# Performance work log

Hardware: AMD Instinct MI355X
Metric: run time of the kernel (lower is better)

Reference implementation:

```python
import jax, jax.numpy as jnp
import numpy as np

S = 2048      # total tokens
DIM = 1024    # model dim
H = 16        # attention heads
DH = 64       # head dim
BOT = 256     # bottleneck dim
NIMG = 4      # images (equal size)
L = S // NIMG # tokens per image
K = 256       # sparse_k
IH = 4        # indexer heads
ID = 16       # indexer head dim
MAXREL = 64   # hardcoded in module
NBUCK = 2 * MAXREL + 1
GH = IH * 2   # gate MLP hidden (expansion=2)


def setup_inputs() -> dict:
    key = jax.random.key(0)
    ks = jax.random.split(key, 16)
    r = lambda i, sh, s=0.02: jax.random.normal(ks[i], sh, jnp.float32) * s
    return dict(
        hidden_states=jax.random.normal(ks[0], (S, DIM), jnp.float32),
        patch_coords=jax.random.randint(ks[1], (S, 2), 0, 64, dtype=jnp.int32),
        cu_seqlens=jnp.arange(NIMG + 1, dtype=jnp.int32) * L,
        rotary_pos_emb=jax.random.uniform(ks[2], (S, DH // 2), jnp.float32) * 3.0,
        Wq_idx=r(3, (2 * IH * ID, DIM)),
        Wk_idx=r(4, (2 * IH * ID, DIM)),
        W1g=r(5, (GH, IH)), b1g=jnp.zeros((GH,), jnp.float32),
        W2g=r(6, (IH, GH)), b2g=jnp.zeros((IH,), jnp.float32),
        rpe_table=r(7, (NBUCK, IH)),
        Wqkv_d=r(8, (BOT, DIM)), bqkv_d=jnp.zeros((BOT,), jnp.float32),
        Wqkv_u=r(9, (3 * DIM, BOT)), bqkv_u=jnp.zeros((3 * DIM,), jnp.float32),
        Wp_d=r(10, (BOT, DIM)), bp_d=jnp.zeros((BOT,), jnp.float32),
        Wp_u=r(11, (DIM, BOT)), bp_u=jnp.zeros((DIM,), jnp.float32),
        scaler=jnp.ones((1,), jnp.float32),
    )


def _rotate_half(x):
    x1, x2 = jnp.split(x, 2, axis=-1)
    return jnp.concatenate([-x2, x1], axis=-1)


def reference(hidden_states, patch_coords, cu_seqlens, rotary_pos_emb,
              Wq_idx, Wk_idx, W1g, b1g, W2g, b2g, rpe_table,
              Wqkv_d, bqkv_d, Wqkv_u, bqkv_u, Wp_d, bp_d, Wp_u, bp_u, scaler):
    n = cu_seqlens.shape[0] - 1            # images (equal size L)
    Li = hidden_states.shape[0] // n
    neg = jnp.finfo(hidden_states.dtype).min

    # QKV via low-rank bottleneck
    qkv = (hidden_states @ Wqkv_d.T + bqkv_d) @ Wqkv_u.T + bqkv_u  # [S, 3*DIM]
    qkv = qkv.reshape(S, 3, H, DH)
    q, k, v = qkv[:, 0], qkv[:, 1], qkv[:, 2]                      # [S, H, DH]

    # vision RoPE (emb = cat(rpe, rpe))
    emb = jnp.concatenate([rotary_pos_emb, rotary_pos_emb], axis=-1)  # [S, DH]
    cos = jnp.cos(emb)[:, None, :]
    sin = jnpp if False else jnp.sin(emb)[:, None, :]
    q = q * cos + _rotate_half(q) * sin
    k = k * cos + _rotate_half(k) * sin

    # ---- interaction indexer, vmapped over equal-size images ----
    xs = hidden_states.reshape(n, Li, DIM)
    pos = patch_coords[:, 1].reshape(n, Li).astype(jnp.float32)
    qI = (xs @ Wq_idx.T).reshape(n, Li, 2 * IH, ID)
    kI = (xs @ Wk_idx.T).reshape(n, Li, 2 * IH, ID)
    dot = jnp.einsum('nqhd,nkhd->nqkh', qI, kI)                    # [n, L, L, 2*IH]
    data_in, gate_in = dot[..., :IH], dot[..., IH:]
    rel = jnp.clip(pos[:, :, None] - pos[:, None, :], -MAXREL, MAXREL)
    bucket = (rel + MAXREL).astype(jnp.int32)                      # [n, L, L]
    rpe = rpe_table[bucket]                                        # [n, L, L, IH]
    relu_scores = jax.nn.relu(data_in + rpe)
    g = jax.nn.sigmoid(jax.nn.relu((gate_in + rpe) @ W1g.T + b1g) @ W2g.T + b2g)
    index_scores = (relu_scores * g).sum(-1)                       # [n, L, L]

    # top-k sparse mask (0 at selected keys, -inf-ish elsewhere)
    _, topk_idx = jax.lax.top_k(index_scores, K)                   # [n, L, K]
    ni = jnp.arange(n)[:, None, None]
    ri = jnp.arange(Li)[None, :, None]
    mask_local = jnp.full((n, Li, Li), neg, hidden_states.dtype).at[ni, ri, topk_idx].set(0.0)

    # block-diagonal full mask
    mask = jnp.full((S, S), neg, hidden_states.dtype)
    for i in range(n):
        mask = mask.at[i * Li:(i + 1) * Li, i * Li:(i + 1) * Li].set(mask_local[i])

    # dense SDPA with additive mask
    att = jnp.einsum('qhd,khd->hqk', q, k) / jnp.sqrt(jnp.float32(DH)).astype(q.dtype)
    att = att + mask[None]
    p = jax.nn.softmax(att, axis=-1)
    out = jnp.einsum('hqk,khd->qhd', p, v).reshape(S, H * DH)

    final = (out @ Wp_d.T + bp_d) @ Wp_u.T + bp_u
    return final * scaler
```

## Files before the change

kernel.cpp:

```cpp
#include <hip/hip_runtime.h>
#include <hip/hip_bf16.h>

#define S_    2048
#define DIM_  1024
#define H_    16
#define DH_   64
#define BOT_  256
#define NIMG_ 4
#define LI_   512
#define K_    256
#define IH_   4
#define ID_   16
#define MAXREL_ 64
#define NBUCK_ 129
#define GH_   8
#define IDH2_ 128

typedef short bf16x8 __attribute__((ext_vector_type(8)));
typedef float f32x4  __attribute__((ext_vector_type(4)));

__device__ __forceinline__ unsigned short f2bf(float x) {
    unsigned u = __float_as_uint(x);
    return (unsigned short)((u + 0x7fffu + ((u >> 16) & 1u)) >> 16);
}
__device__ __forceinline__ float bf2f(unsigned short h) {
    return __uint_as_float(((unsigned)h) << 16);
}

#define OFF_W1_    2097152
#define OFF_WQ_    2359296
#define OFF_WK_    2490368
#define OFF_WQKVU_ 2621440
#define OFF_WPD_   3407872
#define OFF_WPU_   3670016
#define NSPLIT_    3932160

__global__ __launch_bounds__(256) void split_all_kernel(
    const float* __restrict__ hid, const float* __restrict__ wqd,
    const float* __restrict__ wq,  const float* __restrict__ wk,
    const float* __restrict__ wqu, const float* __restrict__ wpd,
    const float* __restrict__ wpu,
    unsigned short* __restrict__ hi, unsigned short* __restrict__ lo)
{
    long e = ((long)blockIdx.x * 256 + threadIdx.x) * 4;
    if (e >= NSPLIT_) return;
    const float* src; long off;
    if (e < OFF_W1_)         { src = hid; off = 0; }
    else if (e < OFF_WQ_)    { src = wqd; off = OFF_W1_; }
    else if (e < OFF_WK_)    { src = wq;  off = OFF_WQ_; }
    else if (e < OFF_WQKVU_) { src = wk;  off = OFF_WK_; }
    else if (e < OFF_WPD_)   { src = wqu; off = OFF_WQKVU_; }
    else if (e < OFF_WPU_)   { src = wpd; off = OFF_WPD_; }
    else                     { src = wpu; off = OFF_WPU_; }
    float4 v = *(const float4*)(src + (e - off));
    ushort4 h, l;
    h.x = f2bf(v.x); l.x = f2bf(v.x - bf2f(h.x));
    h.y = f2bf(v.y); l.y = f2bf(v.y - bf2f(h.y));
    h.z = f2bf(v.z); l.z = f2bf(v.z - bf2f(h.z));
    h.w = f2bf(v.w); l.w = f2bf(v.w - bf2f(h.w));
    *(ushort4*)&hi[e] = h;
    *(ushort4*)&lo[e] = l;
}

__global__ __launch_bounds__(256) void gemm_bf16x3(
    const unsigned short* __restrict__ Ah, const unsigned short* __restrict__ Al,
    const unsigned short* __restrict__ Bh, const unsigned short* __restrict__ Bl,
    const float* __restrict__ bias, const float* __restrict__ scale_ptr,
    float* __restrict__ Cf, int M, int N, int Kd)
{
    __shared__ unsigned short sAh[128 * 40], sAl[128 * 40];
    __shared__ unsigned short sBh[64 * 40],  sBl[64 * 40];
    int tid = threadIdx.x;
    int lane = tid & 63, wv = tid >> 6;
    int wr = wv >> 1, wc = wv & 1;
    int row0 = blockIdx.y * 128, col0 = blockIdx.x * 64;

    f32x4 acc[4][2];
#pragma unroll
    for (int i = 0; i < 4; i++)
#pragma unroll
        for (int j = 0; j < 2; j++) acc[i][j] = (f32x4){0.f, 0.f, 0.f, 0.f};

    int ar = tid >> 1, ac = (tid & 1) * 16;
    int br = tid >> 2, bc = (tid & 3) * 8;
    const unsigned short* gAh = Ah + (size_t)(row0 + ar) * Kd + ac;
    const unsigned short* gAl = Al + (size_t)(row0 + ar) * Kd + ac;
    const unsigned short* gBh = Bh + (size_t)(col0 + br) * Kd + bc;
    const unsigned short* gBl = Bl + (size_t)(col0 + br) * Kd + bc;
    int am = lane & 15, qk = (lane >> 4) * 8;

    for (int k0 = 0; k0 < Kd; k0 += 32) {
        __syncthreads();
        *(float4*)&sAh[ar * 40 + ac]     = *(const float4*)(gAh + k0);
        *(float4*)&sAh[ar * 40 + ac + 8] = *(const float4*)(gAh + k0 + 8);
        *(float4*)&sAl[ar * 40 + ac]     = *(const float4*)(gAl + k0);
        *(float4*)&sAl[ar * 40 + ac + 8] = *(const float4*)(gAl + k0 + 8);
        *(float4*)&sBh[br * 40 + bc]     = *(const float4*)(gBh + k0);
        *(float4*)&sBl[br * 40 + bc]     = *(const float4*)(gBl + k0);
        __syncthreads();

        bf16x8 ah[4], al[4], bh[2], bl[2];
#pragma unroll
        for (int rt = 0; rt < 4; rt++) {
            int r = wr * 64 + rt * 16 + am;
            ah[rt] = *(const bf16x8*)&sAh[r * 40 + qk];
            al[rt] = *(const bf16x8*)&sAl[r * 40 + qk];
        }
#pragma unroll
        for (int ct = 0; ct < 2; ct++) {
            int c = wc * 32 + ct * 16 + am;
            bh[ct] = *(const bf16x8*)&sBh[c * 40 + qk];
            bl[ct] = *(const bf16x8*)&sBl[c * 40 + qk];
        }
#pragma unroll
        for (int rt = 0; rt < 4; rt++)
#pragma unroll
            for (int ct = 0; ct < 2; ct++) {
                acc[rt][ct] = __builtin_amdgcn_mfma_f32_16x16x32_bf16(ah[rt], bh[ct], acc[rt][ct], 0, 0, 0);
                acc[rt][ct] = __builtin_amdgcn_mfma_f32_16x16x32_bf16(ah[rt], bl[ct], acc[rt][ct], 0, 0, 0);
                acc[rt][ct] = __builtin_amdgcn_mfma_f32_16x16x32_bf16(al[rt], bh[ct], acc[rt][ct], 0, 0, 0);
            }
    }

    float scl = scale_ptr ? *scale_ptr : 1.0f;
    int rq = (lane >> 4) * 4;
#pragma unroll
    for (int rt = 0; rt < 4; rt++)
#pragma unroll
        for (int ct = 0; ct < 2; ct++) {
            int col = col0 + wc * 32 + ct * 16 + am;
            float bz = bias ? bias[col] : 0.0f;
#pragma unroll
            for (int rg = 0; rg < 4; rg++) {
                int row = row0 + wr * 64 + rt * 16 + rq + rg;
                Cf[(size_t)row * N + col] = (acc[rt][ct][rg] + bz) * scl;
            }
        }
}

__global__ __launch_bounds__(256) void gemm64_bf16x3(
    const unsigned short* __restrict__ Ah, const unsigned short* __restrict__ Al,
    const unsigned short* __restrict__ Bh, const unsigned short* __restrict__ Bl,
    const float* __restrict__ bias_lo, const float* __restrict__ bias_hi,
    float* __restrict__ Cf, unsigned short* __restrict__ Chi,
    unsigned short* __restrict__ Clo, int M, int N, int Kd, int split_col)
{
    __shared__ unsigned short sAh[64 * 40], sAl[64 * 40];
    __shared__ unsigned short sBh[64 * 40], sBl[64 * 40];
    int tid = threadIdx.x;
    int lane = tid & 63, wv = tid >> 6;
    int wr = wv >> 1, wc = wv & 1;
    int row0 = blockIdx.y * 64, col0 = blockIdx.x * 64;

    f32x4 acc[2][2];
#pragma unroll
    for (int i = 0; i < 2; i++)
#pragma unroll
        for (int j = 0; j < 2; j++) acc[i][j] = (f32x4){0.f, 0.f, 0.f, 0.f};

    int sr = tid >> 2, sc = (tid & 3) * 8;
    const unsigned short* gAh = Ah + (size_t)(row0 + sr) * Kd + sc;
    const unsigned short* gAl = Al + (size_t)(row0 + sr) * Kd + sc;
    const unsigned short* gBh = Bh + (size_t)(col0 + sr) * Kd + sc;
    const unsigned short* gBl = Bl + (size_t)(col0 + sr) * Kd + sc;
    int am = lane & 15, qk = (lane >> 4) * 8;

    for (int k0 = 0; k0 < Kd; k0 += 32) {
        __syncthreads();
        *(float4*)&sAh[sr * 40 + sc] = *(const float4*)(gAh + k0);
        *(float4*)&sAl[sr * 40 + sc] = *(const float4*)(gAl + k0);
        *(float4*)&sBh[sr * 40 + sc] = *(const float4*)(gBh + k0);
        *(float4*)&sBl[sr * 40 + sc] = *(const float4*)(gBl + k0);
        __syncthreads();

        bf16x8 ah[2], al[2], bh[2], bl[2];
#pragma unroll
        for (int rt = 0; rt < 2; rt++) {
            int r = wr * 32 + rt * 16 + am;
            ah[rt] = *(const bf16x8*)&sAh[r * 40 + qk];
            al[rt] = *(const bf16x8*)&sAl[r * 40 + qk];
        }
#pragma unroll
        for (int ct = 0; ct < 2; ct++) {
            int c = wc * 32 + ct * 16 + am;
            bh[ct] = *(const bf16x8*)&sBh[c * 40 + qk];
            bl[ct] = *(const bf16x8*)&sBl[c * 40 + qk];
        }
#pragma unroll
        for (int rt = 0; rt < 2; rt++)
#pragma unroll
            for (int ct = 0; ct < 2; ct++) {
                acc[rt][ct] = __builtin_amdgcn_mfma_f32_16x16x32_bf16(ah[rt], bh[ct], acc[rt][ct], 0, 0, 0);
                acc[rt][ct] = __builtin_amdgcn_mfma_f32_16x16x32_bf16(ah[rt], bl[ct], acc[rt][ct], 0, 0, 0);
                acc[rt][ct] = __builtin_amdgcn_mfma_f32_16x16x32_bf16(al[rt], bh[ct], acc[rt][ct], 0, 0, 0);
            }
    }

    int rq = (lane >> 4) * 4;
#pragma unroll
    for (int rt = 0; rt < 2; rt++)
#pragma unroll
        for (int ct = 0; ct < 2; ct++) {
            int col = col0 + wc * 32 + ct * 16 + am;
#pragma unroll
            for (int rg = 0; rg < 4; rg++) {
                int row = row0 + wr * 32 + rt * 16 + rq + rg;
                float v = acc[rt][ct][rg];
                if (col < split_col) {
                    if (bias_lo) v += bias_lo[col];
                    size_t idx = (size_t)row * split_col + col;
                    unsigned short hh = f2bf(v);
                    Chi[idx] = hh;
                    Clo[idx] = f2bf(v - bf2f(hh));
                } else {
                    if (bias_hi) v += bias_hi[col - split_col];
                    Cf[(size_t)row * (N - split_col) + col - split_col] = v;
                }
            }
        }
}

__global__ __launch_bounds__(256) void rope_kernel(
    float* __restrict__ qkv, const float* __restrict__ rope)
{
    int idx = blockIdx.x * blockDim.x + threadIdx.x;
    if (idx >= S_ * H_ * 32) return;
    int d = idx & 31;
    int h = (idx >> 5) & (H_ - 1);
    int s = idx >> 9;
    float r = rope[s * 32 + d];
    float c = cosf(r), sn = sinf(r);
    size_t base = (size_t)s * 3072 + h * 64 + d;
    float q1 = qkv[base], q2 = qkv[base + 32];
    qkv[base]      = q1 * c - q2 * sn;
    qkv[base + 32] = q2 * c + q1 * sn;
    float k1 = qkv[base + 1024], k2 = qkv[base + 1024 + 32];
    qkv[base + 1024]      = k1 * c - k2 * sn;
    qkv[base + 1024 + 32] = k2 * c + k1 * sn;
}

__global__ __launch_bounds__(256) void score_topk_kernel(
    const float* __restrict__ qIk,
    const int* __restrict__ coords, const float* __restrict__ rpe_table,
    const float* __restrict__ W1g, const float* __restrict__ b1g,
    const float* __restrict__ W2g, const float* __restrict__ b2g,
    unsigned* __restrict__ selmask)
{
    __shared__ float sqI2[4][IDH2_];
    __shared__ unsigned skeys[4][LI_];
    __shared__ int shist[4][256];
    __shared__ float srpe[NBUCK_ * IH_];
    __shared__ float sW1[GH_ * IH_], sb1[GH_], sW2[IH_ * GH_], sb2[IH_];

    int tid  = threadIdx.x;
    int lane = tid & 63;
    int wv   = tid >> 6;
    int row  = blockIdx.x * 4 + wv;
    int n    = (blockIdx.x * 4) >> 9;

    for (int i = tid; i < NBUCK_ * IH_; i += 256) srpe[i] = rpe_table[i];
    if (tid < 32) sW1[tid] = W1g[tid];
    else if (tid < 64) sW2[tid - 32] = W2g[tid - 32];
    else if (tid < 72) sb1[tid - 64] = b1g[tid - 64];
    else if (tid < 76) sb2[tid - 72] = b2g[tid - 72];
    for (int i = tid; i < 4 * IDH2_; i += 256)
        sqI2[i >> 7][i & 127] =
            qIk[(size_t)(blockIdx.x * 4 + (i >> 7)) * 256 + (i & 127)];
    int pq = coords[row * 2 + 1];
    __syncthreads();

    const float* sq = &sqI2[wv][0];
    for (int kt = 0; kt < 8; kt++) {
        int kg   = kt * 64 + lane;
        int krow = n * LI_ + kg;
        const float* kp = qIk + (size_t)krow * 256 + 128;
        float dh[8];
#pragma unroll
        for (int hh = 0; hh < 8; hh++) {
            float acc = 0.0f;
#pragma unroll
            for (int d = 0; d < 16; d += 4) {
                float4 kv = *(const float4*)(kp + hh * 16 + d);
                acc += sq[hh * 16 + d + 0] * kv.x + sq[hh * 16 + d + 1] * kv.y +
                       sq[hh * 16 + d + 2] * kv.z + sq[hh * 16 + d + 3] * kv.w;
            }
            dh[hh] = acc;
        }
        int pk = coords[krow * 2 + 1];
        int rel = pq - pk;
        rel = rel < -MAXREL_ ? -MAXREL_ : (rel > MAXREL_ ? MAXREL_ : rel);
        const float* rp = srpe + (rel + MAXREL_) * IH_;
        float t1[GH_];
#pragma unroll
        for (int g = 0; g < GH_; g++) t1[g] = sb1[g];
#pragma unroll
        for (int j = 0; j < IH_; j++) {
            float gate = dh[IH_ + j] + rp[j];
#pragma unroll
            for (int g = 0; g < GH_; g++) t1[g] += gate * sW1[g * IH_ + j];
        }
#pragma unroll
        for (int g = 0; g < GH_; g++) t1[g] = fmaxf(t1[g], 0.0f);
        float score = 0.0f;
#pragma unroll
        for (int j = 0; j < IH_; j++) {
            float t2 = sb2[j];
#pragma unroll
            for (int g = 0; g < GH_; g++) t2 += t1[g] * sW2[j * GH_ + g];
            float sg = 1.0f / (1.0f + expf(-t2));
            float rs = fmaxf(dh[j] + rp[j], 0.0f);
            score += rs * sg;
        }
        unsigned bits = __float_as_uint(score);
        skeys[wv][kg] = (bits & 0x80000000u) ? ~bits : (bits | 0x80000000u);
    }
    __syncthreads();

    unsigned pref = 0u;
    int kcur = K_;
    const unsigned himask[4] = {0u, 0xFF000000u, 0xFFFF0000u, 0xFFFFFF00u};
#pragma unroll
    for (int pass = 0; pass < 4; pass++) {
        int shift = 24 - pass * 8;
        unsigned hm = himask[pass];
        *(int4*)&shist[wv][4 * lane] = make_int4(0, 0, 0, 0);
        __syncthreads();
#pragma unroll
        for (int c = 0; c < 8; c++) {
            unsigned key = skeys[wv][c * 64 + lane];
            if ((key & hm) == pref) atomicAdd(&shist[wv][(key >> shift) & 255], 1);
        }
        __syncthreads();
        int4 b4 = *(const int4*)&shist[wv][4 * lane];
        int b[4] = {b4.x, b4.y, b4.z, b4.w};
        int t = b[0] + b[1] + b[2] + b[3];
        int Ssum = t;
#pragma unroll
        for (int off = 1; off < 64; off <<= 1) {
            int u = __shfl_down(Ssum, off, 64);
            if (lane + off < 64) Ssum += u;
        }
        int E = Ssum - t;
        int cs[5];
        cs[4] = E;
        cs[3] = b[3] + E;
        cs[2] = b[2] + cs[3];
        cs[1] = b[1] + cs[2];
        cs[0] = b[0] + cs[1];
        bool found = false;
        unsigned cpref = 0u; int ck = 0;
#pragma unroll
        for (int j = 0; j < 4; j++) {
            if (!found && cs[j] >= kcur && cs[j + 1] < kcur) {
                found = true;
                cpref = pref | ((unsigned)(4 * lane + j) << shift);
                ck = kcur - cs[j + 1];
            }
        }
        unsigned long long bm = __ballot(found);
        int src = __ffsll((long long)bm) - 1;
        pref = (unsigned)__shfl((int)cpref, src, 64);
        kcur = __shfl(ck, src, 64);
        __syncthreads();
    }
    unsigned Tu = pref;

    unsigned long long bg[8], be[8];
#pragma unroll
    for (int c = 0; c < 8; c++) {
        unsigned key = skeys[wv][c * 64 + lane];
        bg[c] = __ballot(key > Tu);
        be[c] = __ballot(key == Tu);
    }
    if (lane < 16) {
        int total_gt = 0;
#pragma unroll
        for (int c = 0; c < 8; c++) total_gt += __popcll(bg[c]);
        int base = 0;
#pragma unroll
        for (int c = 0; c < 8; c++) {
            if (2 * c < lane)     base += __popc((unsigned)be[c]);
            if (2 * c + 1 < lane) base += __popc((unsigned)(be[c] >> 32));
        }
        unsigned gw = (unsigned)(bg[lane >> 1] >> (32 * (lane & 1)));
        unsigned ew = (unsigned)(be[lane >> 1] >> (32 * (lane & 1)));
        int ne = K_ - total_gt - base;
        int pc = __popc(ew);
        int m = ne < 0 ? 0 : (ne > pc ? pc : ne);
        while (pc > m) { ew ^= (1u << (31 - __clz(ew))); pc--; }
        selmask[(size_t)row * 16 + lane] = gw | ew;
    }
}

__global__ __launch_bounds__(256) void attn_kernel(
    const float* __restrict__ qkv, const unsigned* __restrict__ selmask,
    unsigned short* __restrict__ outh, unsigned short* __restrict__ outl)
{
    __shared__ unsigned short Qh[64 * 72],  Ql[64 * 72];
    __shared__ unsigned short KPh[64 * 72], KPl[64 * 72];
    __shared__ unsigned short VTh[64 * 72], VTl[64 * 72];
    __shared__ unsigned Ms[64][16];

    int b  = blockIdx.x;
    int qt = b >> 6;
    int nh = b & 63;
    int h  = nh & 15;
    int n  = nh >> 4;
    int tid = threadIdx.x;
    int lane = tid & 63, w = tid >> 6;
    int lane15 = lane & 15, quad = lane >> 4;
    int q0 = n * LI_ + qt * 64;

    for (int i = tid; i < 64 * 16; i += 256)
        Ms[i >> 4][i & 15] = selmask[(size_t)(q0 + (i >> 4)) * 16 + (i & 15)];

    {
        int r = tid >> 2, c0 = (tid & 3) * 16;
        const float* src = qkv + (size_t)(q0 + r) * 3072 + h * 64 + c0;
        unsigned short hb[16], lb[16];
#pragma unroll
        for (int j = 0; j < 16; j += 4) {
            float4 v = *(const float4*)(src + j);
            float f[4] = {v.x * 0.125f, v.y * 0.125f, v.z * 0.125f, v.w * 0.125f};
#pragma unroll
            for (int t = 0; t < 4; t++) {
                unsigned short hh = f2bf(f[t]);
                hb[j + t] = hh;
                lb[j + t] = f2bf(f[t] - bf2f(hh));
            }
        }
        *(uint4*)&Qh[r * 72 + c0]     = *(uint4*)&hb[0];
        *(uint4*)&Qh[r * 72 + c0 + 8] = *(uint4*)&hb[8];
        *(uint4*)&Ql[r * 72 + c0]     = *(uint4*)&lb[0];
        *(uint4*)&Ql[r * 72 + c0 + 8] = *(uint4*)&lb[8];
    }

    f32x4 o_acc[4];
#pragma unroll
    for (int i = 0; i < 4; i++) o_acc[i] = (f32x4){0.f, 0.f, 0.f, 0.f};
    float rsum[4] = {};

    for (int kt = 0; kt < 8; kt++) {
        __syncthreads();
        {
            int r = tid >> 2, c0 = (tid & 3) * 16;
            const float* src = qkv + (size_t)(n * LI_ + kt * 64 + r) * 3072 + 1024 + h * 64 + c0;
            unsigned short hb[16], lb[16];
#pragma unroll
            for (int j = 0; j < 16; j += 4) {
                float4 v = *(const float4*)(src + j);
                float f[4] = {v.x, v.y, v.z, v.w};
#pragma unroll
                for (int t = 0; t < 4; t++) {
                    unsigned short hh = f2bf(f[t]);
                    hb[j + t] = hh;
                    lb[j + t] = f2bf(f[t] - bf2f(hh));
                }
            }
            *(uint4*)&KPh[r * 72 + c0]     = *(uint4*)&hb[0];
            *(uint4*)&KPh[r * 72 + c0 + 8] = *(uint4*)&hb[8];
            *(uint4*)&KPl[r * 72 + c0]     = *(uint4*)&lb[0];
            *(uint4*)&KPl[r * 72 + c0 + 8] = *(uint4*)&lb[8];
        }
        {
            int d = lane;
            int k0 = w * 16;
            const float* src = qkv + (size_t)(n * LI_ + kt * 64 + k0) * 3072 + 2048 + h * 64 + d;
            unsigned short hb[16], lb[16];
#pragma unroll
            for (int j = 0; j < 16; j++) {
                float f = src[(size_t)j * 3072];
                unsigned short hh = f2bf(f);
                hb[j] = hh;
                lb[j] = f2bf(f - bf2f(hh));
            }
            *(uint4*)&VTh[d * 72 + k0]     = *(uint4*)&hb[0];
            *(uint4*)&VTh[d * 72 + k0 + 8] = *(uint4*)&hb[8];
            *(uint4*)&VTl[d * 72 + k0]     = *(uint4*)&lb[0];
            *(uint4*)&VTl[d * 72 + k0 + 8] = *(uint4*)&lb[8];
        }
        __syncthreads();

        f32x4 s_acc[4];
#pragma unroll
        for (int nt = 0; nt < 4; nt++) s_acc[nt] = (f32x4){0.f, 0.f, 0.f, 0.f};
        {
            bf16x8 qfh[2], qfl[2];
#pragma unroll
            for (int ks = 0; ks < 2; ks++) {
                qfh[ks] = *(const bf16x8*)&Qh[(16 * w + lane15) * 72 + ks * 32 + quad * 8];
                qfl[ks] = *(const bf16x8*)&Ql[(16 * w + lane15) * 72 + ks * 32 + quad * 8];
            }
#pragma unroll
            for (int nt = 0; nt < 4; nt++) {
#pragma unroll
                for (int ks = 0; ks < 2; ks++) {
                    bf16x8 kfh = *(const bf16x8*)&KPh[(16 * nt + lane15) * 72 + ks * 32 + quad * 8];
                    bf16x8 kfl = *(const bf16x8*)&KPl[(16 * nt + lane15) * 72 + ks * 32 + quad * 8];
                    s_acc[nt] = __builtin_amdgcn_mfma_f32_16x16x32_bf16(qfh[ks], kfh, s_acc[nt], 0, 0, 0);
                    s_acc[nt] = __builtin_amdgcn_mfma_f32_16x16x32_bf16(qfh[ks], kfl, s_acc[nt], 0, 0, 0);
                    s_acc[nt] = __builtin_amdgcn_mfma_f32_16x16x32_bf16(qfl[ks], kfh, s_acc[nt], 0, 0, 0);
                }
            }
        }
        __syncthreads();

#pragma unroll
        for (int nt = 0; nt < 4; nt++) {
            int kb = kt * 64 + nt * 16 + lane15;
            int wi = kb >> 5, bit = kb & 31;
#pragma unroll
            for (int reg = 0; reg < 4; reg++) {
                int qloc = 16 * w + quad * 4 + reg;
                unsigned mw = Ms[qloc][wi];
                float p = ((mw >> bit) & 1u) ? __expf(s_acc[nt][reg]) : 0.0f;
                rsum[reg] += p;
                unsigned short ph = f2bf(p);
                KPh[qloc * 72 + nt * 16 + lane15] = ph;
                KPl[qloc * 72 + nt * 16 + lane15] = f2bf(p - bf2f(ph));
            }
        }
        __syncthreads();

        {
            bf16x8 pfh[2], pfl[2];
#pragma unroll
            for (int ks = 0; ks < 2; ks++) {
                pfh[ks] = *(const bf16x8*)&KPh[(16 * w + lane15) * 72 + ks * 32 + quad * 8];
                pfl[ks] = *(const bf16x8*)&KPl[(16 * w + lane15) * 72 + ks * 32 + quad * 8];
            }
#pragma unroll
            for (int dt = 0; dt < 4; dt++) {
#pragma unroll
                for (int ks = 0; ks < 2; ks++) {
                    bf16x8 vfh = *(const bf16x8*)&VTh[(16 * dt + lane15) * 72 + ks * 32 + quad * 8];
                    bf16x8 vfl = *(const bf16x8*)&VTl[(16 * dt + lane15) * 72 + ks * 32 + quad * 8];
                    o_acc[dt] = __builtin_amdgcn_mfma_f32_16x16x32_bf16(pfh[ks], vfh, o_acc[dt], 0, 0, 0);
                    o_acc[dt] = __builtin_amdgcn_mfma_f32_16x16x32_bf16(pfh[ks], vfl, o_acc[dt], 0, 0, 0);
                    o_acc[dt] = __builtin_amdgcn_mfma_f32_16x16x32_bf16(pfl[ks], vfh, o_acc[dt], 0, 0, 0);
                }
            }
        }
    }

#pragma unroll
    for (int reg = 0; reg < 4; reg++) {
        rsum[reg] += __shfl_xor(rsum[reg], 1, 64);
        rsum[reg] += __shfl_xor(rsum[reg], 2, 64);
        rsum[reg] += __shfl_xor(rsum[reg], 4, 64);
        rsum[reg] += __shfl_xor(rsum[reg], 8, 64);
    }

#pragma unroll
    for (int dt = 0; dt < 4; dt++) {
#pragma unroll
        for (int reg = 0; reg < 4; reg++) {
            float v = o_acc[dt][reg] / rsum[reg];
            size_t ob = (size_t)(q0 + 16 * w + quad * 4 + reg) * 1024 + h * 64 + 16 * dt + lane15;
            unsigned short hh = f2bf(v);
            outh[ob] = hh;
            outl[ob] = f2bf(v - bf2f(hh));
        }
    }
}

extern "C" void kernel_launch(void* const* d_in, const int* in_sizes, int n_in,
                              void* d_out, int out_size, void* d_ws, size_t ws_size,
                              hipStream_t stream)
{
    const float* hidden  = (const float*)d_in[0];
    const int*   coords  = (const int*)d_in[1];
    const float* rope    = (const float*)d_in[3];
    const float* Wq_idx  = (const float*)d_in[4];
    const float* Wk_idx  = (const float*)d_in[5];
    const float* W1g     = (const float*)d_in[6];
    const float* b1g     = (const float*)d_in[7];
    const float* W2g     = (const float*)d_in[8];
    const float* b2g     = (const float*)d_in[9];
    const float* rpe     = (const float*)d_in[10];
    const float* Wqkv_d  = (const float*)d_in[11];
    const float* bqkv_d  = (const float*)d_in[12];
    const float* Wqkv_u  = (const float*)d_in[13];
    const float* bqkv_u  = (const float*)d_in[14];
    const float* Wp_d    = (const float*)d_in[15];
    const float* bp_d    = (const float*)d_in[16];
    const float* Wp_u    = (const float*)d_in[17];
    const float* bp_u    = (const float*)d_in[18];
    const float* scaler  = (const float*)d_in[19];
    float* out = (float*)d_out;

    unsigned short* sp_hi  = (unsigned short*)d_ws;
    unsigned short* sp_lo  = sp_hi + NSPLIT_;
    unsigned short* mid_hi = sp_lo + NSPLIT_;
    unsigned short* mid_lo = mid_hi + (size_t)S_ * BOT_;
    float* qkv = (float*)(mid_lo + (size_t)S_ * BOT_);
    float* qIk = qkv + (size_t)S_ * 3 * DIM_;
    unsigned* selmask = (unsigned*)(qIk + (size_t)S_ * 256);

    split_all_kernel<<<(NSPLIT_ / 4 + 255) / 256, 256, 0, stream>>>(
        hidden, Wqkv_d, Wq_idx, Wk_idx, Wqkv_u, Wp_d, Wp_u, sp_hi, sp_lo);

    gemm64_bf16x3<<<dim3(512 / 64, S_ / 64), 256, 0, stream>>>(
        sp_hi, sp_lo, sp_hi + OFF_W1_, sp_lo + OFF_W1_,
        bqkv_d, nullptr, qIk, mid_hi, mid_lo, S_, 512, DIM_, 256);

    gemm_bf16x3<<<dim3(3 * DIM_ / 64, S_ / 128), 256, 0, stream>>>(
        mid_hi, mid_lo, sp_hi + OFF_WQKVU_, sp_lo + OFF_WQKVU_,
        bqkv_u, nullptr, qkv, S_, 3 * DIM_, BOT_);

    rope_kernel<<<(S_ * H_ * 32) / 256, 256, 0, stream>>>(qkv, rope);

    score_topk_kernel<<<S_ / 4, 256, 0, stream>>>(
        qIk, coords, rpe, W1g, b1g, W2g, b2g, selmask);

    attn_kernel<<<NIMG_ * H_ * 8, 256, 0, stream>>>(qkv, selmask, sp_hi, sp_lo);

    gemm64_bf16x3<<<dim3(BOT_ / 64, S_ / 64), 256, 0, stream>>>(
        sp_hi, sp_lo, sp_hi + OFF_WPD_, sp_lo + OFF_WPD_,
        bp_d, nullptr, nullptr, mid_hi, mid_lo, S_, BOT_, DIM_, BOT_);

    gemm_bf16x3<<<dim3(DIM_ / 64, S_ / 128), 256, 0, stream>>>(
        mid_hi, mid_lo, sp_hi + OFF_WPU_, sp_lo + OFF_WPU_,
        bp_u, scaler, out, S_, DIM_, BOT_);
}
```

Baseline: 297.0 us.

## Assign one query row per block in score_topk, spreading scoring across all threads

The score/top-k kernel now handles one query row per 256-thread block instead of four rows per block with one wave each. All 256 threads compute the 512 key scores for that row, then only the first wave runs the radix select. Block-wide barriers inside the select loop are removed because only one wave uses the histogram. This quadruples the grid to 2048 blocks and cuts per-thread scoring work, but it also reloads the rpe table and gate weights four times as often and leaves three waves idle during selection.

```diff
diff --git a/kernel.cpp b/kernel.cpp
--- a/kernel.cpp
+++ b/kernel.cpp
@@ -246,32 +246,29 @@
     const float* __restrict__ W2g, const float* __restrict__ b2g,
     unsigned* __restrict__ selmask)
 {
-    __shared__ float sqI2[4][IDH2_];
-    __shared__ unsigned skeys[4][LI_];
-    __shared__ int shist[4][256];
+    __shared__ float sqI[IDH2_];
+    __shared__ unsigned skeys[LI_];
+    __shared__ int hist[256];
     __shared__ float srpe[NBUCK_ * IH_];
     __shared__ float sW1[GH_ * IH_], sb1[GH_], sW2[IH_ * GH_], sb2[IH_];
 
-    int tid  = threadIdx.x;
-    int lane = tid & 63;
-    int wv   = tid >> 6;
-    int row  = blockIdx.x * 4 + wv;
-    int n    = (blockIdx.x * 4) >> 9;
+    int tid = threadIdx.x;
+    int row = blockIdx.x;
+    int n   = row >> 9;
 
     for (int i = tid; i < NBUCK_ * IH_; i += 256) srpe[i] = rpe_table[i];
     if (tid < 32) sW1[tid] = W1g[tid];
     else if (tid < 64) sW2[tid - 32] = W2g[tid - 32];
     else if (tid < 72) sb1[tid - 64] = b1g[tid - 64];
     else if (tid < 76) sb2[tid - 72] = b2g[tid - 72];
-    for (int i = tid; i < 4 * IDH2_; i += 256)
-        sqI2[i >> 7][i & 127] =
-            qIk[(size_t)(blockIdx.x * 4 + (i >> 7)) * 256 + (i & 127)];
+    if (tid < 32)
+        *(float4*)&sqI[tid * 4] = *(const float4*)(qIk + (size_t)row * 256 + tid * 4);
     int pq = coords[row * 2 + 1];
     __syncthreads();
 
-    const float* sq = &sqI2[wv][0];
-    for (int kt = 0; kt < 8; kt++) {
-        int kg   = kt * 64 + lane;
+#pragma unroll 1
+    for (int kk = 0; kk < 2; kk++) {
+        int kg   = kk * 256 + tid;
         int krow = n * LI_ + kg;
         const float* kp = qIk + (size_t)krow * 256 + 128;
         float dh[8];
@@ -281,8 +278,8 @@
 #pragma unroll
             for (int d = 0; d < 16; d += 4) {
                 float4 kv = *(const float4*)(kp + hh * 16 + d);
-                acc += sq[hh * 16 + d + 0] * kv.x + sq[hh * 16 + d + 1] * kv.y +
-                       sq[hh * 16 + d + 2] * kv.z + sq[hh * 16 + d + 3] * kv.w;
+                acc += sqI[hh * 16 + d + 0] * kv.x + sqI[hh * 16 + d + 1] * kv.y +
+                       sqI[hh * 16 + d + 2] * kv.z + sqI[hh * 16 + d + 3] * kv.w;
             }
             dh[hh] = acc;
         }
@@ -312,10 +309,12 @@
             score += rs * sg;
         }
         unsigned bits = __float_as_uint(score);
-        skeys[wv][kg] = (bits & 0x80000000u) ? ~bits : (bits | 0x80000000u);
+        skeys[kg] = (bits & 0x80000000u) ? ~bits : (bits | 0x80000000u);
     }
     __syncthreads();
-
+    if (tid >= 64) return;
+
+    int lane = tid;
     unsigned pref = 0u;
     int kcur = K_;
     const unsigned himask[4] = {0u, 0xFF000000u, 0xFFFF0000u, 0xFFFFFF00u};
@@ -323,15 +322,13 @@
     for (int pass = 0; pass < 4; pass++) {
         int shift = 24 - pass * 8;
         unsigned hm = himask[pass];
-        *(int4*)&shist[wv][4 * lane] = make_int4(0, 0, 0, 0);
-        __syncthreads();
+        *(int4*)&hist[4 * lane] = make_int4(0, 0, 0, 0);
 #pragma unroll
         for (int c = 0; c < 8; c++) {
-            unsigned key = skeys[wv][c * 64 + lane];
-            if ((key & hm) == pref) atomicAdd(&shist[wv][(key >> shift) & 255], 1);
-        }
-        __syncthreads();
-        int4 b4 = *(const int4*)&shist[wv][4 * lane];
+            unsigned key = skeys[c * 64 + lane];
+            if ((key & hm) == pref) atomicAdd(&hist[(key >> shift) & 255], 1);
+        }
+        int4 b4 = *(const int4*)&hist[4 * lane];
         int b[4] = {b4.x, b4.y, b4.z, b4.w};
         int t = b[0] + b[1] + b[2] + b[3];
         int Ssum = t;
@@ -361,14 +358,13 @@
         int src = __ffsll((long long)bm) - 1;
         pref = (unsigned)__shfl((int)cpref, src, 64);
         kcur = __shfl(ck, src, 64);
-        __syncthreads();
     }
     unsigned Tu = pref;
 
     unsigned long long bg[8], be[8];
 #pragma unroll
     for (int c = 0; c < 8; c++) {
-        unsigned key = skeys[wv][c * 64 + lane];
+        unsigned key = skeys[c * 64 + lane];
         bg[c] = __ballot(key > Tu);
         be[c] = __ballot(key == Tu);
     }
@@ -610,7 +606,7 @@
 
     rope_kernel<<<(S_ * H_ * 32) / 256, 256, 0, stream>>>(qkv, rope);
 
-    score_topk_kernel<<<S_ / 4, 256, 0, stream>>>(
+    score_topk_kernel<<<S_, 256, 0, stream>>>(
         qIk, coords, rpe, W1g, b1g, W2g, b2g, selmask);
 
     attn_kernel<<<NIMG_ * H_ * 8, 256, 0, stream>>>(qkv, selmask, sp_hi, sp_lo);
```

After: 324.0 us. +9.1%, slower.
